# Optimization experiments

Measured on AMD Instinct MI355X. Metric: run time of the kernel, lower is better.

## Reference

```python
import jax, jax.numpy as jnp
import numpy as np
from jax import lax

D_MODEL = 1024
D_IN = 1024        # expand=1 -> d_inner = d_model
N_STATE = 16       # d_state
DT_RANK = 64       # ceil(d_model/16)
D_FFN = 4096
BATCH, SEQ = 2, 2048


def setup_inputs() -> dict:
    key = jax.random.key(0)
    ks = jax.random.split(key, 12)
    r = lambda i, shape, s=0.02: jax.random.normal(ks[i], shape, jnp.float32) * s
    ones = lambda n: jnp.ones((n,), jnp.float32)
    zeros = lambda n: jnp.zeros((n,), jnp.float32)
    # S4D-real init for A
    A_log = jnp.log(jnp.tile(jnp.arange(1, N_STATE + 1, dtype=jnp.float32), (D_IN, 1)))
    return {
        "src": jax.random.normal(ks[0], (BATCH, SEQ, D_MODEL), jnp.float32),
        "in_proj_w": r(1, (2 * D_IN, D_MODEL)),
        "conv_w": r(2, (D_IN, 2), 0.5),
        "conv_b": zeros(D_IN),
        "x_proj_w": r(3, (DT_RANK + 2 * N_STATE, D_IN)),
        "dt_proj_w": r(4, (D_IN, DT_RANK), 0.1),
        "dt_proj_b": r(5, (D_IN,), 0.1),
        "A_log": A_log,
        "Dp": ones(D_IN),
        "out_proj_w": r(6, (D_MODEL, D_IN)),
        "mnorm_g": ones(D_MODEL), "mnorm_b": zeros(D_MODEL),
        "n1_g": ones(D_MODEL), "n1_b": zeros(D_MODEL),
        "n2_g": ones(D_MODEL), "n2_b": zeros(D_MODEL),
        "n3_g": ones(D_MODEL), "n3_b": zeros(D_MODEL),
        "ffn_w1": r(7, (D_FFN, D_MODEL)),
        "ffn_w2": r(8, (D_MODEL, D_FFN)),
        "fe_w": r(9, (D_MODEL, D_MODEL)),
        "fe_b": zeros(D_MODEL),
    }


def _ln(x, g, b, eps=1e-5):
    m = x.mean(-1, keepdims=True)
    v = ((x - m) ** 2).mean(-1, keepdims=True)
    return (x - m) / jnp.sqrt(v + eps) * g + b


def _mamba(x, in_proj_w, conv_w, conv_b, x_proj_w, dt_proj_w, dt_proj_b,
           A_log, Dp, out_proj_w):
    B, L, _ = x.shape
    xz = x @ in_proj_w.T                       # (B,L,2*D_IN)
    x_in, z = jnp.split(xz, 2, axis=-1)
    # depthwise causal conv1d, kernel size 2: y[l] = w0*x[l-1] + w1*x[l] + b
    x_prev = jnp.pad(x_in, ((0, 0), (1, 0), (0, 0)))[:, :L]
    x_c = jax.nn.silu(x_prev * conv_w[:, 0] + x_in * conv_w[:, 1] + conv_b)
    x_dbl = x_c @ x_proj_w.T                   # (B,L,DT_RANK+2N)
    dt, Bm, Cm = jnp.split(x_dbl, [DT_RANK, DT_RANK + N_STATE], axis=-1)
    delta = jax.nn.softplus(dt @ dt_proj_w.T + dt_proj_b)   # (B,L,D_IN)
    A = -jnp.exp(A_log)                        # (D_IN,N)
    deltaA = jnp.exp(delta[..., None] * A)                   # (B,L,D_IN,N)
    dBu = delta[..., None] * Bm[:, :, None, :] * x_c[..., None]

    def step(h, t):
        dA_t, dBu_t, C_t = t                   # (B,D_IN,N),(B,D_IN,N),(B,N)
        h = dA_t * h + dBu_t
        y = jnp.einsum('bdn,bn->bd', h, C_t)
        return h, y

    h0 = jnp.zeros((B, D_IN, N_STATE), x.dtype)
    _, ys = lax.scan(step, h0,
                     (deltaA.transpose(1, 0, 2, 3),
                      dBu.transpose(1, 0, 2, 3),
                      Cm.transpose(1, 0, 2)))
    y = ys.transpose(1, 0, 2)                  # (B,L,D_IN)
    y = (y + x_c * Dp) * jax.nn.silu(z)
    return y @ out_proj_w.T


def reference(src, in_proj_w, conv_w, conv_b, x_proj_w, dt_proj_w, dt_proj_b,
              A_log, Dp, out_proj_w, mnorm_g, mnorm_b, n1_g, n1_b, n2_g, n2_b,
              n3_g, n3_b, ffn_w1, ffn_w2, fe_w, fe_b):
    # src1 = MambaBlock(norm1(src)); dropout = identity (eval)
    h = _mamba(_ln(src, n1_g, n1_b), in_proj_w, conv_w, conv_b, x_proj_w,
               dt_proj_w, dt_proj_b, A_log, Dp, out_proj_w)
    src = src + _ln(h, mnorm_g, mnorm_b)
    # FFN: Linear -> LeakyReLU(0.01) -> Linear (no bias)
    f = _ln(src, n2_g, n2_b) @ ffn_w1.T
    f = jnp.where(f >= 0, f, 0.01 * f) @ ffn_w2.T
    src = src + f
    src = src + (_ln(src, n3_g, n3_b) @ fe_w.T + fe_b)
    return src
```

## Files before the change

kernel.cpp:

```cpp
#include <hip/hip_runtime.h>
#include <hip/hip_bf16.h>
#include <cstddef>

#define L_SEQ   2048
#define NBATCH  2
#define NROWS   (NBATCH * L_SEQ)
#define NSTATE  16
#define CH      64
#define NCHUNK  (L_SEQ / CH)

typedef __bf16 bf16x8 __attribute__((ext_vector_type(8)));
typedef float  f32x4  __attribute__((ext_vector_type(4)));
typedef unsigned short u16x4 __attribute__((ext_vector_type(4)));
typedef unsigned short u16x8 __attribute__((ext_vector_type(8)));

static __device__ __forceinline__ unsigned short f2bf(float f) {
  unsigned int x = __builtin_bit_cast(unsigned int, f);
  x += 0x7fffu + ((x >> 16) & 1u);
  return (unsigned short)(x >> 16);
}
static __device__ __forceinline__ float bf2f(unsigned short u) {
  return __builtin_bit_cast(float, ((unsigned int)u) << 16);
}

#define GLDS(g, l) __builtin_amdgcn_global_load_lds( \
    (const __attribute__((address_space(1))) void*)(g), \
    (__attribute__((address_space(3))) void*)(l), 16, 0, 0)

#define DRAIN_VM() asm volatile("s_waitcnt vmcnt(0)" ::: "memory")

__global__ __launch_bounds__(256) void cvt_bf16_kernel(
    const float* __restrict__ in, unsigned short* __restrict__ out, int n4)
{
  const int i = blockIdx.x * 256 + threadIdx.x;
  if (i < n4) {
    const float4 v = reinterpret_cast<const float4*>(in)[i];
    u16x4 o;
    o[0] = f2bf(v.x); o[1] = f2bf(v.y); o[2] = f2bf(v.z); o[3] = f2bf(v.w);
    reinterpret_cast<u16x4*>(out)[i] = o;
  }
}

__global__ __launch_bounds__(256) void cvt_all_kernel(
    const float* __restrict__ ipw, const float* __restrict__ xpw,
    const float* __restrict__ dtw, const float* __restrict__ opw,
    const float* __restrict__ w1,  const float* __restrict__ w2,
    const float* __restrict__ few, float* __restrict__ zx,
    unsigned short* __restrict__ o_ipw, unsigned short* __restrict__ o_xpw,
    unsigned short* __restrict__ o_dtw, unsigned short* __restrict__ o_opw,
    unsigned short* __restrict__ o_w1,  unsigned short* __restrict__ o_w2,
    unsigned short* __restrict__ o_few,
    const float* __restrict__ lsrc, const float* __restrict__ lg,
    const float* __restrict__ lb, unsigned short* __restrict__ louth)
{
  __shared__ float sm[8];
  if (blockIdx.x >= 12832) {
    const int row = blockIdx.x - 12832;
    const int tid = threadIdx.x;
    const float4 v = reinterpret_cast<const float4*>(lsrc + (size_t)row * 1024)[tid];
    float s = v.x + v.y + v.z + v.w;
#pragma unroll
    for (int o = 32; o > 0; o >>= 1) s += __shfl_down(s, o, 64);
    if ((tid & 63) == 0) sm[tid >> 6] = s;
    __syncthreads();
    const float mean = (sm[0] + sm[1] + sm[2] + sm[3]) * (1.f / 1024.f);
    const float dx = v.x - mean, dy = v.y - mean, dz = v.z - mean, dw = v.w - mean;
    float q = dx * dx + dy * dy + dz * dz + dw * dw;
#pragma unroll
    for (int o = 32; o > 0; o >>= 1) q += __shfl_down(q, o, 64);
    __syncthreads();
    if ((tid & 63) == 0) sm[tid >> 6] = q;
    __syncthreads();
    const float var = (sm[0] + sm[1] + sm[2] + sm[3]) * (1.f / 1024.f);
    const float rstd = rsqrtf(var + 1e-5f);
    const float4 gv = reinterpret_cast<const float4*>(lg)[tid];
    const float4 bv = reinterpret_cast<const float4*>(lb)[tid];
    u16x4 ob;
    ob[0] = f2bf(dx * rstd * gv.x + bv.x);
    ob[1] = f2bf(dy * rstd * gv.y + bv.y);
    ob[2] = f2bf(dz * rstd * gv.z + bv.z);
    ob[3] = f2bf(dw * rstd * gv.w + bv.w);
    reinterpret_cast<u16x4*>(louth + (size_t)row * 1024)[tid] = ob;
    return;
  }
  int i = blockIdx.x * 256 + threadIdx.x;
  if (i < 98304) {
    reinterpret_cast<float4*>(zx)[i] = make_float4(0.f, 0.f, 0.f, 0.f);
    return;
  }
  i -= 98304;
  const float* src; unsigned short* dst;
  if (i < 524288)                 { src = ipw; dst = o_ipw; }
  else if ((i -= 524288) < 24576) { src = xpw; dst = o_xpw; }
  else if ((i -= 24576) < 16384)  { src = dtw; dst = o_dtw; }
  else if ((i -= 16384) < 262144) { src = opw; dst = o_opw; }
  else if ((i -= 262144) < 1048576){ src = w1; dst = o_w1; }
  else if ((i -= 1048576) < 1048576){ src = w2; dst = o_w2; }
  else if ((i -= 1048576) < 262144){ src = few; dst = o_few; }
  else return;
  const float4 v = reinterpret_cast<const float4*>(src)[i];
  u16x4 o;
  o[0] = f2bf(v.x); o[1] = f2bf(v.y); o[2] = f2bf(v.z); o[3] = f2bf(v.w);
  reinterpret_cast<u16x4*>(dst)[i] = o;
}

__global__ __launch_bounds__(256) void ln_kernel(
    const float* __restrict__ in, const float* __restrict__ g,
    const float* __restrict__ bta, const float* __restrict__ res,
    float* __restrict__ out, unsigned short* __restrict__ outb)
{
  const int row = blockIdx.x;
  const int tid = threadIdx.x;
  __shared__ float sm[8];
  const float4 v = reinterpret_cast<const float4*>(in + (size_t)row * 1024)[tid];
  float s = v.x + v.y + v.z + v.w;
#pragma unroll
  for (int o = 32; o > 0; o >>= 1) s += __shfl_down(s, o, 64);
  if ((tid & 63) == 0) sm[tid >> 6] = s;
  __syncthreads();
  const float mean = (sm[0] + sm[1] + sm[2] + sm[3]) * (1.f / 1024.f);
  const float dx = v.x - mean, dy = v.y - mean, dz = v.z - mean, dw = v.w - mean;
  float q = dx * dx + dy * dy + dz * dz + dw * dw;
#pragma unroll
  for (int o = 32; o > 0; o >>= 1) q += __shfl_down(q, o, 64);
  __syncthreads();
  if ((tid & 63) == 0) sm[tid >> 6] = q;
  __syncthreads();
  const float var = (sm[0] + sm[1] + sm[2] + sm[3]) * (1.f / 1024.f);
  const float rstd = rsqrtf(var + 1e-5f);
  const float4 gv = reinterpret_cast<const float4*>(g)[tid];
  const float4 bv = reinterpret_cast<const float4*>(bta)[tid];
  float4 o4;
  o4.x = dx * rstd * gv.x + bv.x;
  o4.y = dy * rstd * gv.y + bv.y;
  o4.z = dz * rstd * gv.z + bv.z;
  o4.w = dw * rstd * gv.w + bv.w;
  if (outb) {
    u16x4 ob;
    ob[0] = f2bf(o4.x); ob[1] = f2bf(o4.y); ob[2] = f2bf(o4.z); ob[3] = f2bf(o4.w);
    reinterpret_cast<u16x4*>(outb + (size_t)row * 1024)[tid] = ob;
  } else {
    if (res) {
      const float4 rv = reinterpret_cast<const float4*>(res + (size_t)row * 1024)[tid];
      o4.x += rv.x; o4.y += rv.y; o4.z += rv.z; o4.w += rv.w;
    }
    reinterpret_cast<float4*>(out + (size_t)row * 1024)[tid] = o4;
  }
}

__global__ __launch_bounds__(256) void ln2_kernel(
    const float* __restrict__ in, const float* __restrict__ g1,
    const float* __restrict__ b1, const float* __restrict__ res,
    const float* __restrict__ g2, const float* __restrict__ b2,
    float* __restrict__ out1, unsigned short* __restrict__ out2b)
{
  const int row = blockIdx.x;
  const int tid = threadIdx.x;
  __shared__ float sm[8];
  const float4 v = reinterpret_cast<const float4*>(in + (size_t)row * 1024)[tid];
  float s = v.x + v.y + v.z + v.w;
#pragma unroll
  for (int o = 32; o > 0; o >>= 1) s += __shfl_down(s, o, 64);
  if ((tid & 63) == 0) sm[tid >> 6] = s;
  __syncthreads();
  const float mean = (sm[0] + sm[1] + sm[2] + sm[3]) * (1.f / 1024.f);
  const float dx = v.x - mean, dy = v.y - mean, dz = v.z - mean, dw = v.w - mean;
  float q = dx * dx + dy * dy + dz * dz + dw * dw;
#pragma unroll
  for (int o = 32; o > 0; o >>= 1) q += __shfl_down(q, o, 64);
  __syncthreads();
  if ((tid & 63) == 0) sm[tid >> 6] = q;
  __syncthreads();
  const float var = (sm[0] + sm[1] + sm[2] + sm[3]) * (1.f / 1024.f);
  const float rstd = rsqrtf(var + 1e-5f);
  const float4 g1v = reinterpret_cast<const float4*>(g1)[tid];
  const float4 b1v = reinterpret_cast<const float4*>(b1)[tid];
  const float4 rv = reinterpret_cast<const float4*>(res + (size_t)row * 1024)[tid];
  float4 o4;
  o4.x = dx * rstd * g1v.x + b1v.x + rv.x;
  o4.y = dy * rstd * g1v.y + b1v.y + rv.y;
  o4.z = dz * rstd * g1v.z + b1v.z + rv.z;
  o4.w = dw * rstd * g1v.w + b1v.w + rv.w;
  reinterpret_cast<float4*>(out1 + (size_t)row * 1024)[tid] = o4;
  __syncthreads();
  float s2 = o4.x + o4.y + o4.z + o4.w;
#pragma unroll
  for (int o = 32; o > 0; o >>= 1) s2 += __shfl_down(s2, o, 64);
  if ((tid & 63) == 0) sm[tid >> 6] = s2;
  __syncthreads();
  const float mean2 = (sm[0] + sm[1] + sm[2] + sm[3]) * (1.f / 1024.f);
  const float ex = o4.x - mean2, ey = o4.y - mean2, ez = o4.z - mean2, ew = o4.w - mean2;
  float q2 = ex * ex + ey * ey + ez * ez + ew * ew;
#pragma unroll
  for (int o = 32; o > 0; o >>= 1) q2 += __shfl_down(q2, o, 64);
  __syncthreads();
  if ((tid & 63) == 0) sm[tid >> 6] = q2;
  __syncthreads();
  const float var2 = (sm[0] + sm[1] + sm[2] + sm[3]) * (1.f / 1024.f);
  const float rstd2 = rsqrtf(var2 + 1e-5f);
  const float4 g2v = reinterpret_cast<const float4*>(g2)[tid];
  const float4 b2v = reinterpret_cast<const float4*>(b2)[tid];
  u16x4 ob;
  ob[0] = f2bf(ex * rstd2 * g2v.x + b2v.x);
  ob[1] = f2bf(ey * rstd2 * g2v.y + b2v.y);
  ob[2] = f2bf(ez * rstd2 * g2v.z + b2v.z);
  ob[3] = f2bf(ew * rstd2 * g2v.w + b2v.w);
  reinterpret_cast<u16x4*>(out2b + (size_t)row * 1024)[tid] = ob;
}

__global__ __launch_bounds__(512) void gemm256_kernel(
    const unsigned short* __restrict__ A, int lda,
    const unsigned short* __restrict__ B, int ldb,
    void* __restrict__ Cv, int ldc,
    const float* __restrict__ bias, const float* __restrict__ res,
    int K, int act, int outbf, int gy)
{
  __shared__ __align__(16) unsigned char smem[131072];
  const int t = threadIdx.x;
  const int w = t >> 6, l = t & 63;

  const int q = gridDim.x >> 3;
  const int nid = (blockIdx.x & 7) * q + (blockIdx.x >> 3);
  const int bm = (nid / gy) * 256;
  const int bn = (nid % gy) * 256;

  const int wr = (w >> 2) * 128;
  const int wc = (w & 3) * 64;
  f32x4 acc[8][4] = {};

  const int srow = t >> 3;
  const int sk8 = (t & 7) * 8;
  const unsigned short* gA = A + (size_t)(bm + srow) * lda + sk8;
  const unsigned short* gB = B + (size_t)(bn + srow) * ldb + sk8;

  const int fr = l & 15;
  const int kb = (l >> 4) * 8;

#define SA6(buf) (smem + (buf) * 32768)
#define SB6(buf) (smem + 65536 + (buf) * 32768)

#define STAGE6(buf, k0) do { \
    _Pragma("unroll") \
    for (int ii = 0; ii < 4; ++ii) { \
      GLDS(gA + (k0) + (size_t)(ii * 64) * lda, SA6(buf) + ii * 8192 + w * 1024); \
      GLDS(gB + (k0) + (size_t)(ii * 64) * ldb, SB6(buf) + ii * 8192 + w * 1024); \
    } \
  } while (0)

#define COMPUTE6(buf) do { \
    _Pragma("unroll") \
    for (int s = 0; s < 2; ++s) { \
      bf16x8 af[8], bfr[4]; \
      _Pragma("unroll") \
      for (int j = 0; j < 4; ++j) \
        bfr[j] = *reinterpret_cast<const bf16x8*>((const unsigned short*)SB6(buf) + (wc + j * 16 + fr) * 64 + s * 32 + kb); \
      _Pragma("unroll") \
      for (int i = 0; i < 8; ++i) \
        af[i] = *reinterpret_cast<const bf16x8*>((const unsigned short*)SA6(buf) + (wr + i * 16 + fr) * 64 + s * 32 + kb); \
      _Pragma("unroll") \
      for (int i = 0; i < 8; ++i) \
        _Pragma("unroll") \
        for (int j = 0; j < 4; ++j) \
          acc[i][j] = __builtin_amdgcn_mfma_f32_16x16x32_bf16(af[i], bfr[j], acc[i][j], 0, 0, 0); \
    } \
  } while (0)

  STAGE6(0, 0);
  DRAIN_VM();
  __syncthreads();
  int cur = 0;
  for (int k0 = 64; k0 < K; k0 += 64) {
    __builtin_amdgcn_sched_barrier(0);
    STAGE6(cur ^ 1, k0);
    __builtin_amdgcn_sched_barrier(0);
    COMPUTE6(cur);
    DRAIN_VM();
    __syncthreads();
    cur ^= 1;
  }
  COMPUTE6(cur);
#undef STAGE6
#undef COMPUTE6
#undef SA6
#undef SB6

  const int crow = (l >> 4) * 4;
  const int ccol = l & 15;
  float* Cf = (float*)Cv;
  unsigned short* Cb = (unsigned short*)Cv;
#pragma unroll
  for (int i = 0; i < 8; ++i) {
#pragma unroll
    for (int j = 0; j < 4; ++j) {
      const int n = bn + wc + j * 16 + ccol;
      const float bv = bias ? bias[n] : 0.f;
#pragma unroll
      for (int r = 0; r < 4; ++r) {
        const int m = bm + wr + i * 16 + crow + r;
        float v = acc[i][j][r] + bv;
        if (act == 1) v = (v > 20.f) ? v : __logf(1.f + __expf(v));
        else if (act == 2) v = (v >= 0.f) ? v : 0.01f * v;
        if (res) v += res[(size_t)m * ldc + n];
        if (outbf) Cb[(size_t)m * ldc + n] = f2bf(v);
        else       Cf[(size_t)m * ldc + n] = v;
      }
    }
  }
}

template<int BK>
__global__ __launch_bounds__(512) void gemm_ksplit_kernel(
    const unsigned short* __restrict__ A, int lda,
    const unsigned short* __restrict__ B, int ldb,
    void* __restrict__ Cv, int ldc,
    const float* __restrict__ bias, const float* __restrict__ res,
    int K, int act, int outbf, int gy)
{
  constexpr int ABYTES = 128 * BK * 2;
  constexpr int NISS = (BK == 32) ? 2 : 4;
  constexpr int RPI  = (BK == 32) ? 64 : 32;
  constexpr int NS   = BK / 32;
  __shared__ __align__(16) unsigned char smem[8 * ABYTES];
  const int tid = threadIdx.x;
  const int grp = tid >> 8;
  const int t = tid & 255;
  const int w = t >> 6, l = t & 63;

  const int q = gridDim.x >> 3;
  const int nid = (blockIdx.x & 7) * q + (blockIdx.x >> 3);
  const int bm = (nid / gy) * 128;
  const int bn = (nid % gy) * 128;

  const int K2 = K >> 1;
  const int koff = grp * K2;
  const int wr = (w >> 1) * 64, wc = (w & 1) * 64;
  f32x4 acc[4][4] = {};

  const int srow = (BK == 32) ? (t >> 2) : (t >> 3);
  const int sk   = (BK == 32) ? ((t & 3) * 8) : ((t & 7) * 8);
  const unsigned short* gA = A + (size_t)(bm + srow) * lda + koff + sk;
  const unsigned short* gB = B + (size_t)(bn + srow) * ldb + koff + sk;

  const int gbase = grp * 2 * ABYTES;
  const int fr = l & 15;
  const int kb = (l >> 4) * 8;

#define SAb(buf) (smem + gbase + (buf) * ABYTES)
#define SBb(buf) (smem + 4 * ABYTES + gbase + (buf) * ABYTES)

#define STAGEK(buf, k0) do { \
    _Pragma("unroll") \
    for (int ii = 0; ii < NISS; ++ii) { \
      GLDS(gA + (k0) + (size_t)ii * RPI * lda, SAb(buf) + ii * 4096 + w * 1024); \
      GLDS(gB + (k0) + (size_t)ii * RPI * ldb, SBb(buf) + ii * 4096 + w * 1024); \
    } \
  } while (0)

#define COMPUTEK(buf) do { \
    _Pragma("unroll") \
    for (int s = 0; s < NS; ++s) { \
      bf16x8 af[4], bfr[4]; \
      _Pragma("unroll") \
      for (int i = 0; i < 4; ++i) \
        af[i] = *reinterpret_cast<const bf16x8*>((const unsigned short*)SAb(buf) + (wr + i * 16 + fr) * BK + s * 32 + kb); \
      _Pragma("unroll") \
      for (int j = 0; j < 4; ++j) \
        bfr[j] = *reinterpret_cast<const bf16x8*>((const unsigned short*)SBb(buf) + (wc + j * 16 + fr) * BK + s * 32 + kb); \
      _Pragma("unroll") \
      for (int i = 0; i < 4; ++i) \
        _Pragma("unroll") \
        for (int j = 0; j < 4; ++j) \
          acc[i][j] = __builtin_amdgcn_mfma_f32_16x16x32_bf16(af[i], bfr[j], acc[i][j], 0, 0, 0); \
    } \
  } while (0)

  STAGEK(0, 0);
  DRAIN_VM();
  __syncthreads();
  int cur = 0;
  for (int k0 = BK; k0 < K2; k0 += BK) {
    __builtin_amdgcn_sched_barrier(0);
    STAGEK(cur ^ 1, k0);
    __builtin_amdgcn_sched_barrier(0);
    COMPUTEK(cur);
    DRAIN_VM();
    __syncthreads();
    cur ^= 1;
  }
  COMPUTEK(cur);
#undef STAGEK
#undef COMPUTEK
#undef SAb
#undef SBb

  __syncthreads();
  float* red = (float*)smem;
  if (grp) {
#pragma unroll
    for (int i = 0; i < 4; ++i)
#pragma unroll
      for (int j = 0; j < 4; ++j)
        *reinterpret_cast<f32x4*>(&red[(t << 6) + (i * 4 + j) * 4]) = acc[i][j];
  }
  __syncthreads();
  if (!grp) {
    const int crow = (l >> 4) * 4;
    const int ccol = l & 15;
    float* Cf = (float*)Cv;
    unsigned short* Cb = (unsigned short*)Cv;
#pragma unroll
    for (int i = 0; i < 4; ++i) {
#pragma unroll
      for (int j = 0; j < 4; ++j) {
        const f32x4 o = *reinterpret_cast<const f32x4*>(&red[(t << 6) + (i * 4 + j) * 4]);
        const int n = bn + wc + j * 16 + ccol;
        const float bv = bias ? bias[n] : 0.f;
#pragma unroll
        for (int r = 0; r < 4; ++r) {
          const int m = bm + wr + i * 16 + crow + r;
          float v = acc[i][j][r] + o[r] + bv;
          if (act == 1) v = (v > 20.f) ? v : __logf(1.f + __expf(v));
          else if (act == 2) v = (v >= 0.f) ? v : 0.01f * v;
          if (res) v += res[(size_t)m * ldc + n];
          if (outbf) Cb[(size_t)m * ldc + n] = f2bf(v);
          else       Cf[(size_t)m * ldc + n] = v;
        }
      }
    }
  }
}

__global__ __launch_bounds__(256) void xproj_kernel(
    const unsigned short* __restrict__ A, int lda,
    const unsigned short* __restrict__ B, int ldb,
    float* __restrict__ C)
{
  __shared__ unsigned short As[2][128 * 32];
  __shared__ unsigned short Bs[2][96 * 32];
  const int t = threadIdx.x;
  const int w = t >> 6, l = t & 63;
  const int bm = blockIdx.x * 128;
  const int kbase = blockIdx.y * 128;

  f32x4 acc[2][6] = {};

  const int srow = t >> 2;
  const int sk = (t & 3) * 8;
  const unsigned short* gA0 = A + (size_t)(bm + srow) * lda + kbase + sk;
  const unsigned short* gA1 = gA0 + (size_t)64 * lda;
  const unsigned short* gB0 = B + (size_t)srow * ldb + kbase + sk;
  const unsigned short* gB1 = gB0 + (size_t)64 * ldb;

  const int fr = l & 15;
  const int kb = (l >> 4) * 8;

#define STAGEX(buf, k0) do { \
    GLDS(gA0 + (k0), &As[buf][w * 512]); \
    GLDS(gA1 + (k0), &As[buf][2048 + w * 512]); \
    GLDS(gB0 + (k0), &Bs[buf][w * 512]); \
    if (w < 2) GLDS(gB1 + (k0), &Bs[buf][2048 + w * 512]); \
  } while (0)

#define COMPUTEX(buf) do { \
    bf16x8 af[2], bfr[6]; \
    _Pragma("unroll") \
    for (int i = 0; i < 2; ++i) \
      af[i] = *reinterpret_cast<const bf16x8*>(&As[buf][(w * 32 + i * 16 + fr) * 32 + kb]); \
    _Pragma("unroll") \
    for (int j = 0; j < 6; ++j) \
      bfr[j] = *reinterpret_cast<const bf16x8*>(&Bs[buf][(j * 16 + fr) * 32 + kb]); \
    _Pragma("unroll") \
    for (int i = 0; i < 2; ++i) \
      _Pragma("unroll") \
      for (int j = 0; j < 6; ++j) \
        acc[i][j] = __builtin_amdgcn_mfma_f32_16x16x32_bf16(af[i], bfr[j], acc[i][j], 0, 0, 0); \
  } while (0)

  STAGEX(0, 0);
  DRAIN_VM();
  __syncthreads();
  int cur = 0;
  for (int s = 1; s < 4; ++s) {
    __builtin_amdgcn_sched_barrier(0);
    STAGEX(cur ^ 1, s * 32);
    __builtin_amdgcn_sched_barrier(0);
    COMPUTEX(cur);
    DRAIN_VM();
    __syncthreads();
    cur ^= 1;
  }
  COMPUTEX(cur);
#undef STAGEX
#undef COMPUTEX

  const int crow = (l >> 4) * 4;
  const int ccol = l & 15;
#pragma unroll
  for (int i = 0; i < 2; ++i)
#pragma unroll
    for (int j = 0; j < 6; ++j)
#pragma unroll
      for (int r = 0; r < 4; ++r) {
        const int m = bm + w * 32 + i * 16 + crow + r;
        const int n = j * 16 + ccol;
        atomicAdd(&C[(size_t)m * 96 + n], acc[i][j][r]);
      }
}

__global__ __launch_bounds__(256) void conv_silu_kernel(
    const unsigned short* __restrict__ xz, const float* __restrict__ cw,
    const float* __restrict__ cb, unsigned short* __restrict__ xcb)
{
  const int i = blockIdx.x * 256 + threadIdx.x;
  const int row = i >> 7;
  const int dv = (i & 127) * 8;
  const int l = row & (L_SEQ - 1);
  const u16x8 cur = *reinterpret_cast<const u16x8*>(&xz[(size_t)row * 2048 + dv]);
  u16x8 prev = {};
  if (l != 0) prev = *reinterpret_cast<const u16x8*>(&xz[(size_t)(row - 1) * 2048 + dv]);
  float cwv[16], cbv[8];
#pragma unroll
  for (int qq = 0; qq < 4; ++qq)
    *reinterpret_cast<float4*>(&cwv[qq * 4]) = reinterpret_cast<const float4*>(cw + 2 * dv)[qq];
#pragma unroll
  for (int qq = 0; qq < 2; ++qq)
    *reinterpret_cast<float4*>(&cbv[qq * 4]) = reinterpret_cast<const float4*>(cb + dv)[qq];
  u16x8 o;
#pragma unroll
  for (int e = 0; e < 8; ++e) {
    const float v = bf2f(prev[e]) * cwv[2 * e] + bf2f(cur[e]) * cwv[2 * e + 1] + cbv[e];
    o[e] = f2bf(v / (1.f + __expf(-v)));
  }
  *reinterpret_cast<u16x8*>(&xcb[(size_t)row * 1024 + dv]) = o;
}

__global__ __launch_bounds__(256) void scan_pass1(
    const unsigned short* __restrict__ delta, const unsigned short* __restrict__ xc,
    const float* __restrict__ xdbl, const float* __restrict__ A_log,
    unsigned short* __restrict__ hfin, unsigned short* __restrict__ pcum)
{
  const int tid = threadIdx.x;
  const int db = blockIdx.x & 3;
  const int c = (blockIdx.x >> 2) & (NCHUNK - 1);
  const int b = blockIdx.x >> 7;
  const int d = db * 256 + tid;
  __shared__ float Bsh[CH][16];
  {
    const int lr = tid >> 2, q = tid & 3;
    const float* p = xdbl + ((size_t)(b * L_SEQ + c * CH + lr) * 96) + 64 + q * 4;
    *reinterpret_cast<float4*>(&Bsh[lr][q * 4]) = *reinterpret_cast<const float4*>(p);
  }
  float a[NSTATE];
#pragma unroll
  for (int n = 0; n < NSTATE; ++n) a[n] = -__expf(A_log[d * 16 + n]);
  __syncthreads();
  float h[NSTATE], P[NSTATE];
#pragma unroll
  for (int n = 0; n < NSTATE; ++n) { h[n] = 0.f; P[n] = 1.f; }
  const size_t rowbase = (size_t)(b * L_SEQ + c * CH);
  for (int s = 0; s < CH; ++s) {
    const size_t row = rowbase + s;
    const float dl = bf2f(delta[row * 1024 + d]);
    const float xcv = bf2f(xc[row * 1024 + d]);
#pragma unroll
    for (int n = 0; n < NSTATE; ++n) {
      const float dA = __expf(dl * a[n]);
      h[n] = h[n] * dA + (dl * Bsh[s][n]) * xcv;
      P[n] *= dA;
    }
  }
  const size_t base = ((size_t)((b * NCHUNK + c) * 1024 + d)) * 16;
  u16x8 h0, h1, p0, p1;
#pragma unroll
  for (int n = 0; n < 8; ++n) {
    h0[n] = f2bf(h[n]);     h1[n] = f2bf(h[n + 8]);
    p0[n] = f2bf(P[n]);     p1[n] = f2bf(P[n + 8]);
  }
  *reinterpret_cast<u16x8*>(hfin + base) = h0;
  *reinterpret_cast<u16x8*>(hfin + base + 8) = h1;
  *reinterpret_cast<u16x8*>(pcum + base) = p0;
  *reinterpret_cast<u16x8*>(pcum + base + 8) = p1;
}

__global__ __launch_bounds__(256) void scan_pass2(
    const unsigned short* __restrict__ hfin, const unsigned short* __restrict__ pcum,
    unsigned short* __restrict__ hstart)
{
  const int t = blockIdx.x * 256 + threadIdx.x;
  const int b = t >> 14;
  const int dn = t & 16383;
  const size_t base = (size_t)b * NCHUNK * 16384 + dn;
  float h = 0.f;
  for (int c = 0; c < NCHUNK; ++c) {
    const size_t idx = base + (size_t)c * 16384;
    hstart[idx] = f2bf(h);
    h = bf2f(pcum[idx]) * h + bf2f(hfin[idx]);
  }
}

__global__ __launch_bounds__(256) void scan_pass3(
    const unsigned short* __restrict__ delta, const unsigned short* __restrict__ xc,
    const float* __restrict__ xdbl, const float* __restrict__ A_log,
    const unsigned short* __restrict__ hstart, const float* __restrict__ Dp,
    const unsigned short* __restrict__ xz, unsigned short* __restrict__ yout)
{
  const int tid = threadIdx.x;
  const int db = blockIdx.x & 3;
  const int c = (blockIdx.x >> 2) & (NCHUNK - 1);
  const int b = blockIdx.x >> 7;
  const int d = db * 256 + tid;
  __shared__ float Bsh[CH][16];
  __shared__ float Csh[CH][16];
  {
    const int lr = tid >> 2, q = tid & 3;
    const float* p = xdbl + ((size_t)(b * L_SEQ + c * CH + lr) * 96);
    *reinterpret_cast<float4*>(&Bsh[lr][q * 4]) = *reinterpret_cast<const float4*>(p + 64 + q * 4);
    *reinterpret_cast<float4*>(&Csh[lr][q * 4]) = *reinterpret_cast<const float4*>(p + 80 + q * 4);
  }
  float a[NSTATE];
#pragma unroll
  for (int n = 0; n < NSTATE; ++n) a[n] = -__expf(A_log[d * 16 + n]);
  float h[NSTATE];
  {
    const size_t base = ((size_t)((b * NCHUNK + c) * 1024 + d)) * 16;
    const u16x8 v0 = *reinterpret_cast<const u16x8*>(hstart + base);
    const u16x8 v1 = *reinterpret_cast<const u16x8*>(hstart + base + 8);
#pragma unroll
    for (int n = 0; n < 8; ++n) { h[n] = bf2f(v0[n]); h[n + 8] = bf2f(v1[n]); }
  }
  const float dpv = Dp[d];
  __syncthreads();
  const size_t rowbase = (size_t)(b * L_SEQ + c * CH);
  for (int s = 0; s < CH; ++s) {
    const size_t row = rowbase + s;
    const float dl = bf2f(delta[row * 1024 + d]);
    const float xcv = bf2f(xc[row * 1024 + d]);
    float y = 0.f;
#pragma unroll
    for (int n = 0; n < NSTATE; ++n) {
      const float dA = __expf(dl * a[n]);
      h[n] = h[n] * dA + (dl * Bsh[s][n]) * xcv;
      y += h[n] * Csh[s][n];
    }
    const float z = bf2f(xz[row * 2048 + 1024 + d]);
    const float sil = z / (1.f + __expf(-z));
    yout[row * 1024 + d] = f2bf((y + xcv * dpv) * sil);
  }
}

extern "C" void kernel_launch(void* const* d_in, const int* in_sizes, int n_in,
                              void* d_out, int out_size, void* d_ws, size_t ws_size,
                              hipStream_t stream)
{
  (void)in_sizes; (void)n_in; (void)out_size; (void)ws_size;
  const float* src        = (const float*)d_in[0];
  const float* in_proj_w  = (const float*)d_in[1];
  const float* conv_w     = (const float*)d_in[2];
  const float* conv_b     = (const float*)d_in[3];
  const float* x_proj_w   = (const float*)d_in[4];
  const float* dt_proj_w  = (const float*)d_in[5];
  const float* dt_proj_b  = (const float*)d_in[6];
  const float* A_log      = (const float*)d_in[7];
  const float* Dp         = (const float*)d_in[8];
  const float* out_proj_w = (const float*)d_in[9];
  const float* mnorm_g    = (const float*)d_in[10];
  const float* mnorm_b    = (const float*)d_in[11];
  const float* n1_g       = (const float*)d_in[12];
  const float* n1_b       = (const float*)d_in[13];
  const float* n2_g       = (const float*)d_in[14];
  const float* n2_b       = (const float*)d_in[15];
  const float* n3_g       = (const float*)d_in[16];
  const float* n3_b       = (const float*)d_in[17];
  const float* ffn_w1     = (const float*)d_in[18];
  const float* ffn_w2     = (const float*)d_in[19];
  const float* fe_w       = (const float*)d_in[20];
  const float* fe_b       = (const float*)d_in[21];
  float* out = (float*)d_out;
  float* ws  = (float*)d_ws;

  unsigned short* xzb   = (unsigned short*)ws;
  unsigned short* xdblb = (unsigned short*)(ws + 4194304);
  unsigned short* dtwb  = (unsigned short*)(ws + 4390912);
  unsigned short* deltab= (unsigned short*)(ws + 4423680);
  float* xdbl  = ws + 12582912;
  float* s5    = ws + 17301504;
  float* src1  = ws + 21495808;
  unsigned short* hfin = (unsigned short*)(ws + 25690112);
  unsigned short* pcum = (unsigned short*)(ws + 26738688);
  unsigned short* hst  = (unsigned short*)(ws + 27787264);
  unsigned short* s1b  = (unsigned short*)(ws + 28835840);
  unsigned short* xcb  = (unsigned short*)(ws + 30932992);
  unsigned short* yb   = (unsigned short*)(ws + 33030144);
  unsigned short* f1b  = (unsigned short*)(ws + 35127296);
  unsigned short* ipwb = (unsigned short*)(ws + 43515904);
  unsigned short* xpwb = (unsigned short*)(ws + 44564480);
  unsigned short* opwb = (unsigned short*)(ws + 44613632);
  unsigned short* w1b  = (unsigned short*)(ws + 45137920);
  unsigned short* w2b  = (unsigned short*)(ws + 47235072);
  unsigned short* fewb = (unsigned short*)(ws + 49332224);

  const dim3 blk(256);
  const dim3 blk512(512);

  cvt_all_kernel<<<16928, blk, 0, stream>>>(
      in_proj_w, x_proj_w, dt_proj_w, out_proj_w, ffn_w1, ffn_w2, fe_w, xdbl,
      ipwb, xpwb, dtwb, opwb, w1b, w2b, fewb,
      src, n1_g, n1_b, s1b);

  gemm_ksplit_kernel<32><<<512, blk512, 0, stream>>>(s1b, 1024, ipwb, 1024, xzb, 2048,
                                                     nullptr, nullptr, 1024, 0, 1, 16);
  conv_silu_kernel<<<2048, blk, 0, stream>>>(xzb, conv_w, conv_b, xcb);
  xproj_kernel<<<dim3(32, 8), blk, 0, stream>>>(xcb, 1024, xpwb, 1024, xdbl);
  cvt_bf16_kernel<<<384, blk, 0, stream>>>(xdbl, xdblb, 98304);
  gemm_ksplit_kernel<32><<<256, blk512, 0, stream>>>(xdblb, 96, dtwb, 64, deltab, 1024,
                                                     dt_proj_b, nullptr, 64, 1, 1, 8);
  scan_pass1<<<256, blk, 0, stream>>>(deltab, xcb, xdbl, A_log, hfin, pcum);
  scan_pass2<<<128, blk, 0, stream>>>(hfin, pcum, hst);
  scan_pass3<<<256, blk, 0, stream>>>(deltab, xcb, xdbl, A_log, hst, Dp, xzb, yb);
  gemm_ksplit_kernel<64><<<256, blk512, 0, stream>>>(yb, 1024, opwb, 1024, s5, 1024,
                                                     nullptr, nullptr, 1024, 0, 0, 8);
  ln2_kernel<<<NROWS, blk, 0, stream>>>(s5, mnorm_g, mnorm_b, src,
                                        n2_g, n2_b, src1, s1b);
  gemm256_kernel<<<256, blk512, 0, stream>>>(s1b, 1024, w1b, 1024, f1b, 4096,
                                             nullptr, nullptr, 1024, 2, 1, 16);
  gemm_ksplit_kernel<64><<<256, blk512, 0, stream>>>(f1b, 4096, w2b, 4096, s5, 1024,
                                                     nullptr, src1, 4096, 0, 0, 8);
  ln_kernel<<<NROWS, blk, 0, stream>>>(s5, n3_g, n3_b, nullptr, nullptr, s1b);
  gemm_ksplit_kernel<64><<<256, blk512, 0, stream>>>(s1b, 1024, fewb, 1024, out, 1024,
                                                     fe_b, s5, 1024, 0, 0, 8);
}
```

Before: 378.4 us.

## Use 4-stage K=32 LDS ring with deeper prefetch in 256x256 GEMM

Replaces the double-buffered K=64 tile pipeline with a four-slot ring of K=32 tiles. Three tiles stay in flight, and partial vmcnt waits let global-to-LDS loads overlap several MFMA steps instead of draining fully every iteration. The cost is twice as many barriers per K and smaller compute chunks between syncs. The hand-counted vmcnt values must match the number of GLDS issues per stage exactly, or the kernel will read stale data.

```diff
diff --git a/kernel.cpp b/kernel.cpp
--- a/kernel.cpp
+++ b/kernel.cpp
@@ -228,61 +228,63 @@
   const int wc = (w & 3) * 64;
   f32x4 acc[8][4] = {};
 
-  const int srow = t >> 3;
-  const int sk8 = (t & 7) * 8;
-  const unsigned short* gA = A + (size_t)(bm + srow) * lda + sk8;
-  const unsigned short* gB = B + (size_t)(bn + srow) * ldb + sk8;
+  const int srow = t >> 2;
+  const int sk = (t & 3) * 8;
+  const unsigned short* gA = A + (size_t)(bm + srow) * lda + sk;
+  const unsigned short* gB = B + (size_t)(bn + srow) * ldb + sk;
 
   const int fr = l & 15;
   const int kb = (l >> 4) * 8;
 
-#define SA6(buf) (smem + (buf) * 32768)
-#define SB6(buf) (smem + 65536 + (buf) * 32768)
-
-#define STAGE6(buf, k0) do { \
+#define SA7(s) (smem + (s) * 16384)
+#define SB7(s) (smem + 65536 + (s) * 16384)
+
+#define STAGE7(s, k0) do { \
+    GLDS(gA + (k0), SA7(s) + w * 1024); \
+    GLDS(gA + (k0) + (size_t)128 * lda, SA7(s) + 8192 + w * 1024); \
+    GLDS(gB + (k0), SB7(s) + w * 1024); \
+    GLDS(gB + (k0) + (size_t)128 * ldb, SB7(s) + 8192 + w * 1024); \
+  } while (0)
+
+#define COMPUTE7(s) do { \
+    bf16x8 af[8], bfr[4]; \
     _Pragma("unroll") \
-    for (int ii = 0; ii < 4; ++ii) { \
-      GLDS(gA + (k0) + (size_t)(ii * 64) * lda, SA6(buf) + ii * 8192 + w * 1024); \
-      GLDS(gB + (k0) + (size_t)(ii * 64) * ldb, SB6(buf) + ii * 8192 + w * 1024); \
-    } \
-  } while (0)
-
-#define COMPUTE6(buf) do { \
+    for (int j = 0; j < 4; ++j) \
+      bfr[j] = *reinterpret_cast<const bf16x8*>((const unsigned short*)SB7(s) + (wc + j * 16 + fr) * 32 + kb); \
     _Pragma("unroll") \
-    for (int s = 0; s < 2; ++s) { \
-      bf16x8 af[8], bfr[4]; \
+    for (int i = 0; i < 8; ++i) \
+      af[i] = *reinterpret_cast<const bf16x8*>((const unsigned short*)SA7(s) + (wr + i * 16 + fr) * 32 + kb); \
+    _Pragma("unroll") \
+    for (int i = 0; i < 8; ++i) \
       _Pragma("unroll") \
       for (int j = 0; j < 4; ++j) \
-        bfr[j] = *reinterpret_cast<const bf16x8*>((const unsigned short*)SB6(buf) + (wc + j * 16 + fr) * 64 + s * 32 + kb); \
-      _Pragma("unroll") \
-      for (int i = 0; i < 8; ++i) \
-        af[i] = *reinterpret_cast<const bf16x8*>((const unsigned short*)SA6(buf) + (wr + i * 16 + fr) * 64 + s * 32 + kb); \
-      _Pragma("unroll") \
-      for (int i = 0; i < 8; ++i) \
-        _Pragma("unroll") \
-        for (int j = 0; j < 4; ++j) \
-          acc[i][j] = __builtin_amdgcn_mfma_f32_16x16x32_bf16(af[i], bfr[j], acc[i][j], 0, 0, 0); \
-    } \
+        acc[i][j] = __builtin_amdgcn_mfma_f32_16x16x32_bf16(af[i], bfr[j], acc[i][j], 0, 0, 0); \
   } while (0)
 
-  STAGE6(0, 0);
-  DRAIN_VM();
-  __syncthreads();
-  int cur = 0;
-  for (int k0 = 64; k0 < K; k0 += 64) {
+  const int nt = K >> 5;
+  STAGE7(0, 0);
+  if (nt > 1) STAGE7(1, 32);
+  if (nt > 2) STAGE7(2, 64);
+  if (nt > 2)      asm volatile("s_waitcnt vmcnt(8)" ::: "memory");
+  else if (nt > 1) asm volatile("s_waitcnt vmcnt(4)" ::: "memory");
+  else             asm volatile("s_waitcnt vmcnt(0)" ::: "memory");
+  __builtin_amdgcn_s_barrier();
+  for (int kt = 0; kt < nt; ++kt) {
+    const int s = kt & 3;
     __builtin_amdgcn_sched_barrier(0);
-    STAGE6(cur ^ 1, k0);
+    if (kt + 3 < nt) STAGE7((kt + 3) & 3, (kt + 3) * 32);
     __builtin_amdgcn_sched_barrier(0);
-    COMPUTE6(cur);
-    DRAIN_VM();
-    __syncthreads();
-    cur ^= 1;
-  }
-  COMPUTE6(cur);
-#undef STAGE6
-#undef COMPUTE6
-#undef SA6
-#undef SB6
+    COMPUTE7(s);
+    __builtin_amdgcn_sched_barrier(0);
+    if (kt + 3 < nt)      asm volatile("s_waitcnt vmcnt(8)" ::: "memory");
+    else if (kt + 2 < nt) asm volatile("s_waitcnt vmcnt(4)" ::: "memory");
+    else if (kt + 1 < nt) asm volatile("s_waitcnt vmcnt(0)" ::: "memory");
+    __builtin_amdgcn_s_barrier();
+  }
+#undef STAGE7
+#undef COMPUTE7
+#undef SA7
+#undef SB7
 
   const int crow = (l >> 4) * 4;
   const int ccol = l & 15;
```

After: 375.7 us. About the same (-0.7%).
